# Kernel optimization log

Measured on AMD Instinct MI355X. Metric: run time of the kernel, lower is better.

## Reference

```python
import jax, jax.numpy as jnp
import numpy as np

DIM = 1024
HEADS = 16
HEAD_DIM = DIM // HEADS

def setup_inputs() -> dict:
    key = jax.random.key(0)
    ks = jax.random.split(key, 5)
    x = jax.random.normal(ks[0], (4, 2048, DIM), dtype=jnp.float32)
    s = DIM ** -0.5
    W_qkv = jax.random.normal(ks[1], (DIM, 3 * DIM), dtype=jnp.float32) * s
    b_qkv = jnp.zeros((3 * DIM,), dtype=jnp.float32)
    W_proj = jax.random.normal(ks[2], (DIM, DIM), dtype=jnp.float32) * s
    b_proj = jnp.zeros((DIM,), dtype=jnp.float32)
    return {"x": x, "W_qkv": W_qkv, "b_qkv": b_qkv, "W_proj": W_proj, "b_proj": b_proj}

def reference(x, W_qkv, b_qkv, W_proj, b_proj):
    B, S, D = x.shape
    scale = HEAD_DIM ** -0.5
    qkv = x @ W_qkv + b_qkv                      # [B,S,3D]
    q, k, v = jnp.split(qkv, 3, axis=-1)         # each [B,S,D]
    def heads(t):
        return t.reshape(B, S, HEADS, HEAD_DIM).transpose(0, 2, 1, 3)  # [B,H,S,d]
    q, k, v = heads(q), heads(k), heads(v)
    attn = jnp.einsum('bhqd,bhkd->bhqk', q, k) * scale
    attn = jax.nn.softmax(attn, axis=-1)
    out = jnp.einsum('bhqk,bhkd->bhqd', attn, v)  # [B,H,S,d]
    out = out.transpose(0, 2, 1, 3).reshape(B, S, D)
    return out @ W_proj + b_proj
```

## Files before the change

### kernel.cpp

```cpp
#include <hip/hip_runtime.h>
#include <hip/hip_bf16.h>
#include <cstdint>


#define SEQ   2048
#define NDIM  1024
#define HEADS 16
#define HD    64

typedef __attribute__((ext_vector_type(8))) short bf16x8;
typedef __attribute__((ext_vector_type(4))) float f32x4;

typedef __attribute__((address_space(1))) void glob_void;
typedef __attribute__((address_space(3))) void lds_void;

__device__ __forceinline__ float b2f(short s) {
    return __uint_as_float(((uint32_t)(uint16_t)s) << 16);
}
__device__ __forceinline__ short f2b(float f) {
    uint32_t u = __float_as_uint(f);
    u += 0x7FFF + ((u >> 16) & 1);
    return (short)(u >> 16);
}
__device__ __forceinline__ uint32_t pk2(float a, float b) {
    return (uint32_t)(uint16_t)f2b(a) | ((uint32_t)(uint16_t)f2b(b) << 16);
}
__device__ __forceinline__ uint32_t cvtpk(float lo, float hi) {
    uint32_t d;
    asm("v_cvt_pk_bf16_f32 %0, %1, %2" : "=v"(d) : "v"(lo), "v"(hi));
    return d;
}

__global__ __launch_bounds__(256) void sentinel_k(float* __restrict__ out, float v, int n) {
    const int i = blockIdx.x * 256 + threadIdx.x;
    if (i < n) out[i] = v;
}

__global__ __launch_bounds__(256) void transpose_k(const float* __restrict__ W,
                                                   short* __restrict__ WT,
                                                   int R, int C) {
    __shared__ short t[32][33];
    const int bx = blockIdx.x * 32;
    const int by = blockIdx.y * 32;
    const int tx = threadIdx.x, ty = threadIdx.y;
#pragma unroll
    for (int i = 0; i < 32; i += 8)
        t[ty + i][tx] = f2b(W[(size_t)(by + ty + i) * C + bx + tx]);
    __syncthreads();
#pragma unroll
    for (int i = 0; i < 32; i += 8)
        WT[(size_t)(bx + ty + i) * R + by + tx] = t[tx][ty + i];
}

__global__ __launch_bounds__(256) void gemm_bt(const void* __restrict__ A,
                                               const short* __restrict__ BT,
                                               const float* __restrict__ bias,
                                               void* __restrict__ Cout,
                                               int N, int K, int lda,
                                               int amode, int cmode) {
    __shared__ short As[128 * 64];
    __shared__ short Bs[128 * 64];

    const short* Ab = (const short*)A;
    const float* Af = (const float*)A;

    const int tid  = threadIdx.x;
    const int lane = tid & 63;
    const int wid  = tid >> 6;
    const int ln16 = lane & 15;
    const int quad = lane >> 4;
    const int wm = (wid & 1) * 64;
    const int wn = (wid >> 1) * 64;
    const int bm = blockIdx.y * 128;
    const int bn = blockIdx.x * 128;

    f32x4 acc[4][4];
#pragma unroll
    for (int i = 0; i < 4; ++i)
#pragma unroll
        for (int j = 0; j < 4; ++j) {
            acc[i][j][0] = 0.f; acc[i][j][1] = 0.f; acc[i][j][2] = 0.f; acc[i][j][3] = 0.f;
        }

    const int rbase = tid >> 3;
    const int k8    = (tid & 7) * 8;

    for (int ks = 0; ks < K; ks += 64) {
        __syncthreads();
#pragma unroll
        for (int i = 0; i < 4; ++i) {
            const int row = i * 32 + rbase;
            const int c   = i * 256 + tid;
            const short* gb = BT + (size_t)(bn + row) * K + ks + k8;
            __builtin_amdgcn_global_load_lds((glob_void*)gb, (lds_void*)(Bs + c * 8), 16, 0, 0);
        }
        if (amode) {
#pragma unroll
            for (int i = 0; i < 4; ++i) {
                const int row = i * 32 + rbase;
                const int c   = i * 256 + tid;
                const short* ga = Ab + (size_t)(bm + row) * lda + ks + k8;
                __builtin_amdgcn_global_load_lds((glob_void*)ga, (lds_void*)(As + c * 8), 16, 0, 0);
            }
        } else {
#pragma unroll
            for (int i = 0; i < 4; ++i) {
                const int row = i * 32 + rbase;
                const int c   = i * 256 + tid;
                const float* ga = Af + (size_t)(bm + row) * lda + ks + k8;
                const float4 f0 = *(const float4*)ga;
                const float4 f1 = *(const float4*)(ga + 4);
                union { bf16x8 v; short s[8]; } u;
                u.s[0] = f2b(f0.x); u.s[1] = f2b(f0.y); u.s[2] = f2b(f0.z); u.s[3] = f2b(f0.w);
                u.s[4] = f2b(f1.x); u.s[5] = f2b(f1.y); u.s[6] = f2b(f1.z); u.s[7] = f2b(f1.w);
                *(bf16x8*)(As + c * 8) = u.v;
            }
        }
        __syncthreads();

#pragma unroll
        for (int kk = 0; kk < 2; ++kk) {
            bf16x8 a[4], b[4];
#pragma unroll
            for (int t = 0; t < 4; ++t) {
                a[t] = *(const bf16x8*)(As + (wm + t * 16 + ln16) * 64 + kk * 32 + quad * 8);
                b[t] = *(const bf16x8*)(Bs + (wn + t * 16 + ln16) * 64 + kk * 32 + quad * 8);
            }
#pragma unroll
            for (int tm = 0; tm < 4; ++tm)
#pragma unroll
                for (int tn = 0; tn < 4; ++tn)
                    acc[tm][tn] = __builtin_amdgcn_mfma_f32_16x16x32_bf16(a[tm], b[tn], acc[tm][tn], 0, 0, 0);
        }
    }

#pragma unroll
    for (int tm = 0; tm < 4; ++tm) {
        const int row = bm + wm + tm * 16 + quad * 4;
#pragma unroll
        for (int tn = 0; tn < 4; ++tn) {
            const int col = bn + wn + tn * 16 + ln16;
            const float bv = bias[col];
#pragma unroll
            for (int r = 0; r < 4; ++r) {
                const float cv = acc[tm][tn][r] + bv;
                const size_t idx = (size_t)(row + r) * N + col;
                if (cmode) ((float*)Cout)[idx] = cv;
                else       ((short*)Cout)[idx] = f2b(cv);
            }
        }
    }
}

__global__ __launch_bounds__(256, 3) void attn_k(short* qkv) {
    __shared__ __attribute__((aligned(16))) char smem[49152];
    short*    Ks   = (short*)smem;
    uint32_t* VTw  = (uint32_t*)(smem + 16384);
    uint32_t* Psw  = (uint32_t*)(smem + 32768);
    short*    Ps   = (short*)(smem + 32768);
    float*    Obuf = (float*)smem;
    float*    lred = (float*)(smem + 32768);

    const int tid  = threadIdx.x;
    const int lane = tid & 63;
    const int wid  = tid >> 6;
    const int ln16 = lane & 15;
    const int quad = lane >> 4;
    const int sw   = ln16 & 7;

    const int bx = blockIdx.x;
    const int qt = bx & 31;
    const int bh = bx >> 5;
    const int b  = bh >> 4;
    const int h  = bh & 15;
    const int q0 = qt * 64;

    const size_t row0 = ((size_t)b * SEQ) * 3072 + h * HD;

#pragma unroll
    for (int i = 0; i < 2; ++i) {
        const int c   = i * 256 + tid;
        const int r   = c >> 3;
        const int col = (c ^ r) & 7;
        __builtin_amdgcn_global_load_lds(
            (glob_void*)(qkv + row0 + (size_t)(q0 + r) * 3072 + col * 8),
            (lds_void*)(Ps + c * 8), 16, 0, 0);
    }
    __syncthreads();
    bf16x8 qf[4][2];
#pragma unroll
    for (int qg = 0; qg < 4; ++qg) {
        const short* qb = Ps + (qg * 16 + ln16) * 64;
        qf[qg][0] = *(const bf16x8*)(qb + ((quad ^ sw) << 3));
        qf[qg][1] = *(const bf16x8*)(qb + (((4 + quad) ^ sw) << 3));
    }
    __syncthreads();

    float l[4] = {0.f, 0.f, 0.f, 0.f};
    f32x4 o[4][4];
#pragma unroll
    for (int t = 0; t < 4; ++t)
#pragma unroll
        for (int qg = 0; qg < 4; ++qg) {
            o[t][qg][0] = 0.f; o[t][qg][1] = 0.f; o[t][qg][2] = 0.f; o[t][qg][3] = 0.f;
        }

    const int vp   = tid & 63;
    const int vd16 = (tid >> 6) * 16;
    const int slab = wid * 32;

    const float C1 = 0.18033688f;
    const float C0 = -17.3123405f;

    for (int kb = 0; kb < SEQ; kb += 128) {
        __syncthreads();
#pragma unroll
        for (int i = 0; i < 4; ++i) {
            const int c   = i * 256 + tid;
            const int r   = c >> 3;
            const int col = (c ^ r) & 7;
            __builtin_amdgcn_global_load_lds(
                (glob_void*)(qkv + row0 + (size_t)(kb + r) * 3072 + 1024 + col * 8),
                (lds_void*)(Ks + c * 8), 16, 0, 0);
        }
        {
            const short* gv = qkv + row0 + (size_t)(kb + 2 * vp) * 3072 + 2048 + vd16;
            union { uint4 u; uint32_t w[4]; } a0, a1, b0, b1;
            a0.u = *(const uint4*)gv;
            a1.u = *(const uint4*)(gv + 8);
            b0.u = *(const uint4*)(gv + 3072);
            b1.u = *(const uint4*)(gv + 3072 + 8);
#pragma unroll
            for (int j = 0; j < 8; ++j) {
                const uint32_t sel = (j & 1) ? 0x07060302u : 0x05040100u;
                const int wsw = vp ^ (j << 2);
                VTw[(vd16 + j) * 64 + wsw]     = __builtin_amdgcn_perm(b0.w[j >> 1], a0.w[j >> 1], sel);
                VTw[(vd16 + 8 + j) * 64 + wsw] = __builtin_amdgcn_perm(b1.w[j >> 1], a1.w[j >> 1], sel);
            }
        }
        __syncthreads();

#pragma unroll
        for (int kg = 0; kg < 2; ++kg) {
            const short* kb_ = Ks + (slab + kg * 16 + ln16) * 64;
            const bf16x8 a0 = *(const bf16x8*)(kb_ + ((quad ^ sw) << 3));
            const bf16x8 a1 = *(const bf16x8*)(kb_ + (((4 + quad) ^ sw) << 3));
#pragma unroll
            for (int qg = 0; qg < 4; ++qg) {
                f32x4 z; z[0] = 0.f; z[1] = 0.f; z[2] = 0.f; z[3] = 0.f;
                z = __builtin_amdgcn_mfma_f32_16x16x32_bf16(a0, qf[qg][0], z, 0, 0, 0);
                z = __builtin_amdgcn_mfma_f32_16x16x32_bf16(a1, qf[qg][1], z, 0, 0, 0);
                const float p0 = __builtin_amdgcn_exp2f(fmaf(z[0], C1, C0));
                const float p1 = __builtin_amdgcn_exp2f(fmaf(z[1], C1, C0));
                const float p2 = __builtin_amdgcn_exp2f(fmaf(z[2], C1, C0));
                const float p3 = __builtin_amdgcn_exp2f(fmaf(z[3], C1, C0));
                l[qg] += (p0 + p1) + (p2 + p3);
                const int prow = qg * 16 + ln16;
                const int wb   = wid * 16 + kg * 8 + quad * 2;
                uint2 pv;
                pv.x = cvtpk(p0, p1);
                pv.y = cvtpk(p2, p3);
                *(uint2*)(Psw + prow * 64 + (wb ^ (sw << 2))) = pv;
            }
        }

        bf16x8 bp[4];
#pragma unroll
        for (int qg = 0; qg < 4; ++qg) {
            const int prow = qg * 16 + ln16;
            bp[qg] = *(const bf16x8*)(Psw + prow * 64 + ((wid * 16 + quad * 4) ^ (sw << 2)));
        }
#pragma unroll
        for (int t = 0; t < 4; ++t) {
            const bf16x8 av = *(const bf16x8*)(VTw + (t * 16 + ln16) * 64
                                               + ((wid * 16 + quad * 4) ^ (sw << 2)));
#pragma unroll
            for (int qg = 0; qg < 4; ++qg)
                o[t][qg] = __builtin_amdgcn_mfma_f32_16x16x32_bf16(av, bp[qg], o[t][qg], 0, 0, 0);
        }
    }

    __syncthreads();
#pragma unroll
    for (int qg = 0; qg < 4; ++qg) {
        l[qg] += __shfl_xor(l[qg], 16, 64);
        l[qg] += __shfl_xor(l[qg], 32, 64);
    }
    if (quad == 0) {
#pragma unroll
        for (int qg = 0; qg < 4; ++qg)
            lred[wid * 64 + qg * 16 + ln16] = l[qg];
    }
    for (int w = 0; w < 4; ++w) {
        if (wid == w) {
#pragma unroll
            for (int t = 0; t < 4; ++t)
#pragma unroll
                for (int qg = 0; qg < 4; ++qg) {
                    float* dst = &Obuf[(qg * 16 + ln16) * 68 + t * 16 + quad * 4];
                    if (w == 0) {
                        *(f32x4*)dst = o[t][qg];
                    } else {
                        f32x4 prev = *(const f32x4*)dst;
                        prev[0] += o[t][qg][0]; prev[1] += o[t][qg][1];
                        prev[2] += o[t][qg][2]; prev[3] += o[t][qg][3];
                        *(f32x4*)dst = prev;
                    }
                }
        }
        __syncthreads();
    }

    const int q  = tid & 63;
    const int dc = (tid >> 6) * 16;
    const float linv = 1.0f / (lred[q] + lred[64 + q] + lred[128 + q] + lred[192 + q]);
    const float* ob = Obuf + q * 68 + dc;
    const f32x4 o0 = *(const f32x4*)ob;
    const f32x4 o1 = *(const f32x4*)(ob + 4);
    const f32x4 o2 = *(const f32x4*)(ob + 8);
    const f32x4 o3 = *(const f32x4*)(ob + 12);
    union { uint4 u[2]; uint32_t w[8]; } outp;
    outp.w[0] = cvtpk(o0[0] * linv, o0[1] * linv);
    outp.w[1] = cvtpk(o0[2] * linv, o0[3] * linv);
    outp.w[2] = cvtpk(o1[0] * linv, o1[1] * linv);
    outp.w[3] = cvtpk(o1[2] * linv, o1[3] * linv);
    outp.w[4] = cvtpk(o2[0] * linv, o2[1] * linv);
    outp.w[5] = cvtpk(o2[2] * linv, o2[3] * linv);
    outp.w[6] = cvtpk(o3[0] * linv, o3[1] * linv);
    outp.w[7] = cvtpk(o3[2] * linv, o3[3] * linv);
    uint4* dst = (uint4*)(qkv + row0 + (size_t)(q0 + q) * 3072 + dc);
    dst[0] = outp.u[0];
    dst[1] = outp.u[1];
}

extern "C" void kernel_launch(void* const* d_in, const int* in_sizes, int n_in,
                              void* d_out, int out_size, void* d_ws, size_t ws_size,
                              hipStream_t stream) {
    const float* x     = (const float*)d_in[0];
    const float* Wqkv  = (const float*)d_in[1];
    const float* bqkv  = (const float*)d_in[2];
    const float* Wproj = (const float*)d_in[3];
    const float* bproj = (const float*)d_in[4];
    float* out = (float*)d_out;

    int bad = -1;
    if (n_in != 5) bad = 9;
    else {
        const int want[5] = {8388608, 3145728, 3072, 1048576, 1024};
        for (int i = 0; i < 5; ++i) if (in_sizes[i] != want[i]) { bad = i; break; }
        if (bad < 0 && out_size != 8388608) bad = 8;
    }
    if (bad >= 0) {
        sentinel_k<<<(out_size + 255) / 256, 256, 0, stream>>>(out, 1000.0f + 100.0f * bad, out_size);
        return;
    }

    char* ws = (char*)d_ws;
    short* wqkvT  = (short*)(ws);
    short* wprojT = (short*)(ws + 6291456);
    short* qkv    = (short*)(ws + 8388608);

    transpose_k<<<dim3(96, 32), dim3(32, 8), 0, stream>>>(Wqkv, wqkvT, 1024, 3072);
    transpose_k<<<dim3(32, 32), dim3(32, 8), 0, stream>>>(Wproj, wprojT, 1024, 1024);

    gemm_bt<<<dim3(3072 / 128, 8192 / 128), 256, 0, stream>>>(
        x, wqkvT, bqkv, qkv, 3072, 1024, 1024, 0, 0);

    attn_k<<<dim3(4 * HEADS * (SEQ / 64)), 256, 0, stream>>>(qkv);

    gemm_bt<<<dim3(1024 / 128, 8192 / 128), 256, 0, stream>>>(
        qkv, wprojT, bproj, out, 1024, 1024, 3072, 1, 1);
}
```

Baseline: 335.4 us.

## Make attention LDS use wave-local, load Q/K straight to registers, prefetch V

The attention kernel stops staging Q and K tiles through shared memory and instead loads each wave's MFMA fragments directly from global memory into registers. The V transpose buffer is re-swizzled so each wave only reads the V^T and P data it wrote itself, which allows both per-iteration block barriers to be dropped. V for the next key block is prefetched into registers during the current block's QK^T/softmax phase, and s_setprio raises priority around the PV MFMAs. Shared memory drops from 48KB to 32KB, which may allow more resident blocks, but the direct global K loads are narrower and less coalesced than the previous async LDS copies.

```diff
diff --git a/kernel.cpp b/kernel.cpp
--- a/kernel.cpp
+++ b/kernel.cpp
@@ -14,16 +14,10 @@
 typedef __attribute__((address_space(1))) void glob_void;
 typedef __attribute__((address_space(3))) void lds_void;
 
-__device__ __forceinline__ float b2f(short s) {
-    return __uint_as_float(((uint32_t)(uint16_t)s) << 16);
-}
 __device__ __forceinline__ short f2b(float f) {
     uint32_t u = __float_as_uint(f);
     u += 0x7FFF + ((u >> 16) & 1);
     return (short)(u >> 16);
-}
-__device__ __forceinline__ uint32_t pk2(float a, float b) {
-    return (uint32_t)(uint16_t)f2b(a) | ((uint32_t)(uint16_t)f2b(b) << 16);
 }
 __device__ __forceinline__ uint32_t cvtpk(float lo, float hi) {
     uint32_t d;
@@ -153,13 +147,11 @@
 }
 
 __global__ __launch_bounds__(256, 3) void attn_k(short* qkv) {
-    __shared__ __attribute__((aligned(16))) char smem[49152];
-    short*    Ks   = (short*)smem;
-    uint32_t* VTw  = (uint32_t*)(smem + 16384);
-    uint32_t* Psw  = (uint32_t*)(smem + 32768);
-    short*    Ps   = (short*)(smem + 32768);
+    __shared__ __attribute__((aligned(16))) char smem[32768];
+    uint32_t* VTw  = (uint32_t*)smem;
+    uint32_t* Psw  = (uint32_t*)(smem + 16384);
     float*    Obuf = (float*)smem;
-    float*    lred = (float*)(smem + 32768);
+    float*    lred = (float*)(smem + 17408);
 
     const int tid  = threadIdx.x;
     const int lane = tid & 63;
@@ -176,25 +168,15 @@
     const int q0 = qt * 64;
 
     const size_t row0 = ((size_t)b * SEQ) * 3072 + h * HD;
-
-#pragma unroll
-    for (int i = 0; i < 2; ++i) {
-        const int c   = i * 256 + tid;
-        const int r   = c >> 3;
-        const int col = (c ^ r) & 7;
-        __builtin_amdgcn_global_load_lds(
-            (glob_void*)(qkv + row0 + (size_t)(q0 + r) * 3072 + col * 8),
-            (lds_void*)(Ps + c * 8), 16, 0, 0);
-    }
-    __syncthreads();
+    const int slab = wid * 32;
+
     bf16x8 qf[4][2];
 #pragma unroll
     for (int qg = 0; qg < 4; ++qg) {
-        const short* qb = Ps + (qg * 16 + ln16) * 64;
-        qf[qg][0] = *(const bf16x8*)(qb + ((quad ^ sw) << 3));
-        qf[qg][1] = *(const bf16x8*)(qb + (((4 + quad) ^ sw) << 3));
-    }
-    __syncthreads();
+        const short* qr = qkv + row0 + (size_t)(q0 + qg * 16 + ln16) * 3072 + quad * 8;
+        qf[qg][0] = *(const bf16x8*)(qr);
+        qf[qg][1] = *(const bf16x8*)(qr + 32);
+    }
 
     float l[4] = {0.f, 0.f, 0.f, 0.f};
     f32x4 o[4][4];
@@ -205,46 +187,43 @@
             o[t][qg][0] = 0.f; o[t][qg][1] = 0.f; o[t][qg][2] = 0.f; o[t][qg][3] = 0.f;
         }
 
-    const int vp   = tid & 63;
-    const int vd16 = (tid >> 6) * 16;
-    const int slab = wid * 32;
+    const int vpair = wid * 16 + ln16;
+    const int vd16  = quad * 16;
+    const short* kbase = qkv + row0 + (size_t)(slab + ln16) * 3072 + 1024 + quad * 8;
+    const short* vbase = qkv + row0 + 2048 + vd16;
 
     const float C1 = 0.18033688f;
     const float C0 = -17.3123405f;
 
+    union U4 { uint4 u; uint32_t w[4]; };
+    U4 va0, va1, vb0, vb1;
+    {
+        const short* gv = vbase + (size_t)(2 * vpair) * 3072;
+        va0.u = *(const uint4*)gv;
+        va1.u = *(const uint4*)(gv + 8);
+        vb0.u = *(const uint4*)(gv + 3072);
+        vb1.u = *(const uint4*)(gv + 3072 + 8);
+    }
+
     for (int kb = 0; kb < SEQ; kb += 128) {
-        __syncthreads();
-#pragma unroll
-        for (int i = 0; i < 4; ++i) {
-            const int c   = i * 256 + tid;
-            const int r   = c >> 3;
-            const int col = (c ^ r) & 7;
-            __builtin_amdgcn_global_load_lds(
-                (glob_void*)(qkv + row0 + (size_t)(kb + r) * 3072 + 1024 + col * 8),
-                (lds_void*)(Ks + c * 8), 16, 0, 0);
-        }
-        {
-            const short* gv = qkv + row0 + (size_t)(kb + 2 * vp) * 3072 + 2048 + vd16;
-            union { uint4 u; uint32_t w[4]; } a0, a1, b0, b1;
-            a0.u = *(const uint4*)gv;
-            a1.u = *(const uint4*)(gv + 8);
-            b0.u = *(const uint4*)(gv + 3072);
-            b1.u = *(const uint4*)(gv + 3072 + 8);
-#pragma unroll
-            for (int j = 0; j < 8; ++j) {
-                const uint32_t sel = (j & 1) ? 0x07060302u : 0x05040100u;
-                const int wsw = vp ^ (j << 2);
-                VTw[(vd16 + j) * 64 + wsw]     = __builtin_amdgcn_perm(b0.w[j >> 1], a0.w[j >> 1], sel);
-                VTw[(vd16 + 8 + j) * 64 + wsw] = __builtin_amdgcn_perm(b1.w[j >> 1], a1.w[j >> 1], sel);
-            }
-        }
-        __syncthreads();
+        const short* kr = kbase + (size_t)kb * 3072;
+        const bf16x8 kf0 = *(const bf16x8*)(kr);
+        const bf16x8 kf1 = *(const bf16x8*)(kr + 32);
+        const bf16x8 kf2 = *(const bf16x8*)(kr + 16 * 3072);
+        const bf16x8 kf3 = *(const bf16x8*)(kr + 16 * 3072 + 32);
+
+#pragma unroll
+        for (int j = 0; j < 8; ++j) {
+            const uint32_t sel = (j & 1) ? 0x07060302u : 0x05040100u;
+            const int wsw = vpair ^ (j << 2) ^ (quad << 4);
+            VTw[(vd16 + j) * 64 + wsw]     = __builtin_amdgcn_perm(vb0.w[j >> 1], va0.w[j >> 1], sel);
+            VTw[(vd16 + 8 + j) * 64 + wsw] = __builtin_amdgcn_perm(vb1.w[j >> 1], va1.w[j >> 1], sel);
+        }
 
 #pragma unroll
         for (int kg = 0; kg < 2; ++kg) {
-            const short* kb_ = Ks + (slab + kg * 16 + ln16) * 64;
-            const bf16x8 a0 = *(const bf16x8*)(kb_ + ((quad ^ sw) << 3));
-            const bf16x8 a1 = *(const bf16x8*)(kb_ + (((4 + quad) ^ sw) << 3));
+            const bf16x8 a0 = kg ? kf2 : kf0;
+            const bf16x8 a1 = kg ? kf3 : kf1;
 #pragma unroll
             for (int qg = 0; qg < 4; ++qg) {
                 f32x4 z; z[0] = 0.f; z[1] = 0.f; z[2] = 0.f; z[3] = 0.f;
@@ -264,20 +243,29 @@
             }
         }
 
+        {
+            const int kb2 = (kb + 128) & (SEQ - 1);
+            const short* gv = vbase + (size_t)(kb2 + 2 * vpair) * 3072;
+            va0.u = *(const uint4*)gv;
+            va1.u = *(const uint4*)(gv + 8);
+            vb0.u = *(const uint4*)(gv + 3072);
+            vb1.u = *(const uint4*)(gv + 3072 + 8);
+        }
+
         bf16x8 bp[4];
 #pragma unroll
-        for (int qg = 0; qg < 4; ++qg) {
-            const int prow = qg * 16 + ln16;
-            bp[qg] = *(const bf16x8*)(Psw + prow * 64 + ((wid * 16 + quad * 4) ^ (sw << 2)));
-        }
+        for (int qg = 0; qg < 4; ++qg)
+            bp[qg] = *(const bf16x8*)(Psw + (qg * 16 + ln16) * 64 + ((wid * 16 + quad * 4) ^ (sw << 2)));
+        __builtin_amdgcn_s_setprio(1);
 #pragma unroll
         for (int t = 0; t < 4; ++t) {
             const bf16x8 av = *(const bf16x8*)(VTw + (t * 16 + ln16) * 64
-                                               + ((wid * 16 + quad * 4) ^ (sw << 2)));
+                                               + ((wid * 16 + quad * 4) ^ (sw << 2) ^ (t << 4)));
 #pragma unroll
             for (int qg = 0; qg < 4; ++qg)
                 o[t][qg] = __builtin_amdgcn_mfma_f32_16x16x32_bf16(av, bp[qg], o[t][qg], 0, 0, 0);
         }
+        __builtin_amdgcn_s_setprio(0);
     }
 
     __syncthreads();
```

Measured after the change: 345.5 us. +3.0%, slower.

## Pre-convert x to bf16 and remap GEMM workgroups across XCDs

Applied to the files above, without the earlier changes.

Adds a separate pass that converts the fp32 input x to bf16 in workspace, so the QKV GEMM reads bf16 A tiles (amode 1) instead of converting fp32 on every tile load. This halves the A-operand traffic, which each tile is re-read by many column blocks. It also remaps the GEMM block index so consecutive workgroups are spread in strides of eight, aiming at better L2 locality across the MI355X's chiplets. The cost is an extra kernel launch and a 16 MB workspace write and read, and the bf16 path only runs if the workspace is large enough.

```diff
diff --git a/kernel.cpp b/kernel.cpp
--- a/kernel.cpp
+++ b/kernel.cpp
@@ -14,17 +14,11 @@
 typedef __attribute__((address_space(1))) void glob_void;
 typedef __attribute__((address_space(3))) void lds_void;
 
-__device__ __forceinline__ float b2f(short s) {
-    return __uint_as_float(((uint32_t)(uint16_t)s) << 16);
-}
 __device__ __forceinline__ short f2b(float f) {
     uint32_t u = __float_as_uint(f);
     u += 0x7FFF + ((u >> 16) & 1);
     return (short)(u >> 16);
 }
-__device__ __forceinline__ uint32_t pk2(float a, float b) {
-    return (uint32_t)(uint16_t)f2b(a) | ((uint32_t)(uint16_t)f2b(b) << 16);
-}
 __device__ __forceinline__ uint32_t cvtpk(float lo, float hi) {
     uint32_t d;
     asm("v_cvt_pk_bf16_f32 %0, %1, %2" : "=v"(d) : "v"(lo), "v"(hi));
@@ -34,6 +28,18 @@
 __global__ __launch_bounds__(256) void sentinel_k(float* __restrict__ out, float v, int n) {
     const int i = blockIdx.x * 256 + threadIdx.x;
     if (i < n) out[i] = v;
+}
+
+__global__ __launch_bounds__(256) void convert_k(const float* __restrict__ in,
+                                                 short* __restrict__ out, int n8) {
+    const int i = blockIdx.x * 256 + threadIdx.x;
+    if (i >= n8) return;
+    const float4 f0 = *(const float4*)(in + (size_t)i * 8);
+    const float4 f1 = *(const float4*)(in + (size_t)i * 8 + 4);
+    union { bf16x8 v; short s[8]; } u;
+    u.s[0] = f2b(f0.x); u.s[1] = f2b(f0.y); u.s[2] = f2b(f0.z); u.s[3] = f2b(f0.w);
+    u.s[4] = f2b(f1.x); u.s[5] = f2b(f1.y); u.s[6] = f2b(f1.z); u.s[7] = f2b(f1.w);
+    *(bf16x8*)(out + (size_t)i * 8) = u.v;
 }
 
 __global__ __launch_bounds__(256) void transpose_k(const float* __restrict__ W,
@@ -71,8 +77,14 @@
     const int quad = lane >> 4;
     const int wm = (wid & 1) * 64;
     const int wn = (wid >> 1) * 64;
-    const int bm = blockIdx.y * 128;
-    const int bn = blockIdx.x * 128;
+
+    const int nbx = gridDim.x;
+    const int nwg = gridDim.x * gridDim.y;
+    int lin = blockIdx.y * nbx + blockIdx.x;
+    if ((nwg & 7) == 0)
+        lin = (lin & 7) * (nwg >> 3) + (lin >> 3);
+    const int bm = (lin / nbx) * 128;
+    const int bn = (lin % nbx) * 128;
 
     f32x4 acc[4][4];
 #pragma unroll
@@ -359,12 +371,20 @@
     short* wqkvT  = (short*)(ws);
     short* wprojT = (short*)(ws + 6291456);
     short* qkv    = (short*)(ws + 8388608);
+    short* xb     = (short*)(ws + 58720256);
+    const bool have_xb = (ws_size >= 58720256ull + 16777216ull);
 
     transpose_k<<<dim3(96, 32), dim3(32, 8), 0, stream>>>(Wqkv, wqkvT, 1024, 3072);
     transpose_k<<<dim3(32, 32), dim3(32, 8), 0, stream>>>(Wproj, wprojT, 1024, 1024);
 
-    gemm_bt<<<dim3(3072 / 128, 8192 / 128), 256, 0, stream>>>(
-        x, wqkvT, bqkv, qkv, 3072, 1024, 1024, 0, 0);
+    if (have_xb) {
+        convert_k<<<4096, 256, 0, stream>>>(x, xb, 1048576);
+        gemm_bt<<<dim3(3072 / 128, 8192 / 128), 256, 0, stream>>>(
+            xb, wqkvT, bqkv, qkv, 3072, 1024, 1024, 1, 0);
+    } else {
+        gemm_bt<<<dim3(3072 / 128, 8192 / 128), 256, 0, stream>>>(
+            x, wqkvT, bqkv, qkv, 3072, 1024, 1024, 0, 0);
+    }
 
     attn_k<<<dim3(4 * HEADS * (SEQ / 64)), 256, 0, stream>>>(qkv);
 
```

Result: faster. 320.5 us (-4.4%).
